# Performance work log

Hardware: AMD Instinct MI355X
Metric: run time of the kernel (lower is better)

Reference implementation:

```python
import jax, jax.numpy as jnp
import numpy as np

N = 10000
E = 160000
H = 4
NEG_SLOPE = 0.2


def _edge_softmax(e, dst):
    # e: [E, H] logits; softmax over edges sharing the same dst node
    m = jax.ops.segment_max(e, dst, num_segments=N)          # [N, H]
    m = jnp.where(jnp.isfinite(m), m, 0.0)
    ex = jnp.exp(e - m[dst])                                  # [E, H]
    den = jax.ops.segment_sum(ex, dst, num_segments=N)       # [N, H]
    return ex / (den[dst] + 1e-9)


def _gat_layer(x, src, dst, W, al, ar, resW, edge=None, We=None, ae=None):
    # x: [N, Fin]; W: [Fin, H, D]; al/ar/ae: [H, D]; resW: [Fin, D]
    feat = jnp.einsum('ni,ihd->nhd', x, W)                    # [N, H, D]
    el = jnp.einsum('nhd,hd->nh', feat, al)                   # [N, H]
    er = jnp.einsum('nhd,hd->nh', feat, ar)                   # [N, H]
    e = el[src] + er[dst]                                     # [E, H]
    if edge is not None:
        ef = jnp.einsum('ei,ihd->ehd', edge, We)              # [E, H, D]
        e = e + jnp.einsum('ehd,hd->eh', ef, ae)
    e = jax.nn.leaky_relu(e, NEG_SLOPE)
    alpha = _edge_softmax(e, dst)                             # [E, H]
    msg = feat[src] * alpha[:, :, None]                       # [E, H, D]
    out = jax.ops.segment_sum(msg, dst, num_segments=N)      # [N, H, D]
    return out.mean(axis=1) + x @ resW                        # [N, D]


def setup_inputs() -> dict:
    key = jax.random.key(0)
    ks = jax.random.split(key, 24)
    node_in, edge_in, hid, out = 128, 64, 128, 256
    s = 0.1
    d = {
        'node_feats': jax.random.normal(ks[0], (N, node_in), jnp.float32),
        'edge_feats': jax.random.normal(ks[1], (E, edge_in), jnp.float32),
        'src': jax.random.randint(ks[2], (E,), 0, N, jnp.int32),
        'dst': jax.random.randint(ks[3], (E,), 0, N, jnp.int32),
        # conv1 (with edge feats): node_in -> hid
        'W1':  s * jax.random.normal(ks[4],  (node_in, H, hid), jnp.float32),
        'We1': s * jax.random.normal(ks[5],  (edge_in, H, hid), jnp.float32),
        'al1': s * jax.random.normal(ks[6],  (H, hid), jnp.float32),
        'ar1': s * jax.random.normal(ks[7],  (H, hid), jnp.float32),
        'ae1': s * jax.random.normal(ks[8],  (H, hid), jnp.float32),
        'res1': s * jax.random.normal(ks[9], (node_in, hid), jnp.float32),
        # conv2: hid -> hid
        'W2':  s * jax.random.normal(ks[10], (hid, H, hid), jnp.float32),
        'al2': s * jax.random.normal(ks[11], (H, hid), jnp.float32),
        'ar2': s * jax.random.normal(ks[12], (H, hid), jnp.float32),
        'res2': s * jax.random.normal(ks[13], (hid, hid), jnp.float32),
        # conv3: hid -> hid
        'W3':  s * jax.random.normal(ks[14], (hid, H, hid), jnp.float32),
        'al3': s * jax.random.normal(ks[15], (H, hid), jnp.float32),
        'ar3': s * jax.random.normal(ks[16], (H, hid), jnp.float32),
        'res3': s * jax.random.normal(ks[17], (hid, hid), jnp.float32),
        # conv4: hid -> out
        'W4':  s * jax.random.normal(ks[18], (hid, H, out), jnp.float32),
        'al4': s * jax.random.normal(ks[19], (H, out), jnp.float32),
        'ar4': s * jax.random.normal(ks[20], (H, out), jnp.float32),
        'res4': s * jax.random.normal(ks[21], (hid, out), jnp.float32),
    }
    return d


def reference(node_feats, edge_feats, src, dst,
              W1, We1, al1, ar1, ae1, res1,
              W2, al2, ar2, res2,
              W3, al3, ar3, res3,
              W4, al4, ar4, res4):
    h = jax.nn.relu(_gat_layer(node_feats, src, dst, W1, al1, ar1, res1,
                               edge=edge_feats, We=We1, ae=ae1))
    h = jax.nn.relu(_gat_layer(h, src, dst, W2, al2, ar2, res2))
    h = jax.nn.relu(_gat_layer(h, src, dst, W3, al3, ar3, res3))
    h = jax.nn.relu(_gat_layer(h, src, dst, W4, al4, ar4, res4))
    return h
```

## Files before the change

kernel.cpp:

```cpp
#include <hip/hip_runtime.h>

#define NN 10000
#define EE 160000

typedef __attribute__((ext_vector_type(8))) short bf16x8;
typedef __attribute__((ext_vector_type(4))) float f32x4;
typedef __attribute__((ext_vector_type(2))) float f32x2;

__device__ __forceinline__ float b2f(unsigned short s) {
    union { unsigned u; float f; } v; v.u = ((unsigned)s) << 16; return v.f;
}
__device__ __forceinline__ short f2b(float f) {
    union { float f; unsigned u; } v; v.f = f;
    unsigned r = v.u + 0x7FFF + ((v.u >> 16) & 1);
    return (short)(r >> 16);
}
__device__ __forceinline__ unsigned char f2q(float f) {
    return (unsigned char)(__builtin_amdgcn_cvt_pk_fp8_f32(f, f, 0, false) & 0xFF);
}

__global__ __launch_bounds__(256) void scan_kernel(const int* __restrict__ counts,
                                                   int* __restrict__ off,
                                                   int* __restrict__ cur, int n) {
    __shared__ int part[256];
// ... 14 lines not shown
        r[q] = v;
        s += v.x + v.y + v.z + v.w;
    }
    part[tid] = s;
    __syncthreads();
    for (int o = 1; o < 256; o <<= 1) {
        int v = (tid >= o) ? part[tid - o] : 0;
        __syncthreads();
        part[tid] += v;
        __syncthreads();
    }
    int run = tid ? part[tid - 1] : 0;
    #pragma unroll
    for (int q = 0; q < 10; ++q) {
        int4 v = r[q], o4;
        o4.x = run; run += v.x;
        o4.y = run; run += v.y;
        o4.z = run; run += v.z;
        o4.w = run; run += v.w;
        int idx = lo + q * 4;
        if (idx + 3 < n) { *(int4*)(off + idx) = o4; *(int4*)(cur + idx) = o4; }
        else if (idx < n) {
            off[idx] = o4.x; cur[idx] = o4.x;
            if (idx + 1 < n) { off[idx + 1] = o4.y; cur[idx + 1] = o4.y; }
            if (idx + 2 < n) { off[idx + 2] = o4.z; cur[idx + 2] = o4.z; }
        }
    }
    if (tid == 255) off[n] = part[255];
}

__global__ __launch_bounds__(256) void fill_extra(const int* __restrict__ src,
                                                  const int* __restrict__ dst,
                                                  int* __restrict__ cur,
                                                  const float* __restrict__ ef,
                                                  const float* __restrict__ vbuf,
                                                  int* __restrict__ ssrc,
                                                  float* __restrict__ extra, int E) {
    __shared__ float vs[256];
    vs[threadIdx.x] = vbuf[threadIdx.x];
    __syncthreads();
    int e = blockIdx.x * 256 + threadIdx.x;
    if (e >= E) return;
    int p = atomicAdd(&cur[dst[e]], 1);
    ssrc[p] = src[e];
    float a0 = 0.f, a1 = 0.f, a2 = 0.f, a3 = 0.f;
    const float4* e4 = (const float4*)(ef + (size_t)e * 64);
    #pragma unroll
    for (int c = 0; c < 16; ++c) {
        float4 x = e4[c];
        int b = c * 16;
        a0 += x.x * vs[b + 0] + x.y * vs[b + 4] + x.z * vs[b + 8] + x.w * vs[b + 12];
        a1 += x.x * vs[b + 1] + x.y * vs[b + 5] + x.z * vs[b + 9] + x.w * vs[b + 13];
        a2 += x.x * vs[b + 2] + x.y * vs[b + 6] + x.z * vs[b + 10] + x.w * vs[b + 14];
        a3 += x.x * vs[b + 3] + x.y * vs[b + 7] + x.z * vs[b + 11] + x.w * vs[b + 15];
    }
    float4 o; o.x = a0; o.y = a1; o.z = a2; o.w = a3;
    *(float4*)(extra + (size_t)p * 4) = o;
}

struct PrepParams {
    const float* tsrc[8];
    short* tdst[8];
    int tN[8];
    int tshift[8];
    int tcum4[9];
    const float* W[4]; const float* al[4]; const float* ar[4];
    short* Wc[4]; int Dl[4]; int base[4];
    const float* We1; const float* ae1; float* vbuf;
    const float* node_feats; short* xb;
    int* counts;
    int bWA, bV, bC, bZ;
};
__global__ __launch_bounds__(256) void prep_kernel(PrepParams P) {
    int blk = blockIdx.x, tid = threadIdx.x;
    if (blk < P.bWA) {
        int t = blk * 256 + tid;
        if (t >= P.tcum4[8]) return;
        int i = 0;
        #pragma unroll
        for (int j = 1; j < 8; ++j) i += (t >= P.tcum4[j]);
        int local = t - P.tcum4[i];
        int N = P.tN[i], sh = P.tshift[i];
        int k = local >> (sh - 2);
        int nq = local & ((N >> 2) - 1);
        float4 v = *(const float4*)(P.tsrc[i] + (size_t)k * N + nq * 4);
        short* d = P.tdst[i] + (size_t)nq * 4 * 128 + k;
        d[0] = f2b(v.x); d[128] = f2b(v.y); d[256] = f2b(v.z); d[384] = f2b(v.w);
    } else if (blk < P.bV) {
        int bl = blk - P.bWA;
        int l = bl >> 7, within = bl & 127;
// ... 76 lines not shown
            int gm = m0 + mt * 16 + r;
            bf16x8 afrag = {};
            if (gm < M) afrag = *(const bf16x8*)(A + (size_t)gm * 128 + k0 + quad * 8);
            acc[mt] = __builtin_amdgcn_mfma_f32_16x16x32_bf16(afrag, bfrag, acc[mt], 0, 0, 0);
        }
    }
    int col = n0 + r;
    #pragma unroll
    for (int mt = 0; mt < 4; ++mt) {
        #pragma unroll
        for (int rr = 0; rr < 4; ++rr) {
            int gm = m0 + mt * 16 + quad * 4 + rr;
            if (gm >= M) continue;
            float v = acc[mt][rr];
            if (col < HD)              featq[(size_t)gm * HD + col] = f2q(v);
            else if (col < HD + D)     y[(size_t)gm * D + (col - HD)] = v;
            else if (col < HD + D + 8) elr[(size_t)gm * 8 + (col - HD - D)] = v;
        }
    }
}

template <int D>
__global__ __launch_bounds__(256) void gemm_fused(const short* __restrict__ A,
                                                  const short* __restrict__ Bt,
                                                  unsigned char* __restrict__ featq,
                                                  float* __restrict__ y,
                                                  float* __restrict__ elr,
                                                  int M) {
    gemm_body<D>(A, Bt, featq, y, elr, M, blockIdx.x, blockIdx.y);
}

__global__ __launch_bounds__(256) void hist_gemm1(const int* __restrict__ dst,
                                                  int* __restrict__ counts,
                                                  const short* __restrict__ A,
                                                  const short* __restrict__ Bt,
                                                  unsigned char* __restrict__ featq,
                                                  float* __restrict__ y,
                                                  float* __restrict__ elr) {
    constexpr int HB = (EE + 255) / 256;
    if (blockIdx.x < HB) {
        int e = blockIdx.x * 256 + threadIdx.x;
        if (e < EE) atomicAdd(&counts[dst[e]], 1);
        return;
    }
    int b = blockIdx.x - HB;
    gemm_body<128>(A, Bt, featq, y, elr, NN, b % 11, b / 11);
}

__device__ __forceinline__ void accum16q(float* a, uint4 v, float w) {
    f32x2 p;
    p = __builtin_amdgcn_cvt_pk_f32_fp8(v.x, false); a[0] += w * p.x; a[1] += w * p.y;
    p = __builtin_amdgcn_cvt_pk_f32_fp8(v.x, true);  a[2] += w * p.x; a[3] += w * p.y;
    p = __builtin_amdgcn_cvt_pk_f32_fp8(v.y, false); a[4] += w * p.x; a[5] += w * p.y;
    p = __builtin_amdgcn_cvt_pk_f32_fp8(v.y, true);  a[6] += w * p.x; a[7] += w * p.y;
    p = __builtin_amdgcn_cvt_pk_f32_fp8(v.z, false); a[8] += w * p.x; a[9] += w * p.y;
    p = __builtin_amdgcn_cvt_pk_f32_fp8(v.z, true);  a[10] += w * p.x; a[11] += w * p.y;
    p = __builtin_amdgcn_cvt_pk_f32_fp8(v.w, false); a[12] += w * p.x; a[13] += w * p.y;
    p = __builtin_amdgcn_cvt_pk_f32_fp8(v.w, true);  a[14] += w * p.x; a[15] += w * p.y;
}

__device__ __forceinline__ float hsel(int h, float s0, float s1, float s2, float s3) {
    return h == 0 ? s0 : h == 1 ? s1 : h == 2 ? s2 : s3;
}

__device__ __forceinline__ void gather128(int T, int deg, int sub, int h, int sidx,
                                          float e0, float e1, float e2, float e3,
                                          const unsigned char* __restrict__ basep,
                                          float acc[16]) {
    int it = 0;
    for (; it + 4 <= T; it += 4) {
        int j0 = 4 * it + sub, j1 = j0 + 4, j2 = j0 + 8, j3 = j0 + 12;
        int c0 = j0 < deg ? j0 : deg - 1;
        int c1 = j1 < deg ? j1 : deg - 1;
        int c2 = j2 < deg ? j2 : deg - 1;
        int c3 = j3 < deg ? j3 : deg - 1;
        float m0 = j0 < deg ? 1.f : 0.f, m1 = j1 < deg ? 1.f : 0.f;
        float m2 = j2 < deg ? 1.f : 0.f, m3 = j3 < deg ? 1.f : 0.f;
        int s0 = __shfl(sidx, c0), s1 = __shfl(sidx, c1);
        int s2 = __shfl(sidx, c2), s3 = __shfl(sidx, c3);
        uint4 v0 = *(const uint4*)(basep + (size_t)s0 * 512);
        uint4 v1 = *(const uint4*)(basep + (size_t)s1 * 512);
        uint4 v2 = *(const uint4*)(basep + (size_t)s2 * 512);
        uint4 v3 = *(const uint4*)(basep + (size_t)s3 * 512);
        float w0 = hsel(h, __shfl(e0, c0), __shfl(e1, c0), __shfl(e2, c0), __shfl(e3, c0)) * m0;
        float w1 = hsel(h, __shfl(e0, c1), __shfl(e1, c1), __shfl(e2, c1), __shfl(e3, c1)) * m1;
        float w2 = hsel(h, __shfl(e0, c2), __shfl(e1, c2), __shfl(e2, c2), __shfl(e3, c2)) * m2;
        float w3 = hsel(h, __shfl(e0, c3), __shfl(e1, c3), __shfl(e2, c3), __shfl(e3, c3)) * m3;
        accum16q(acc, v0, w0); accum16q(acc, v1, w1);
        accum16q(acc, v2, w2); accum16q(acc, v3, w3);
    }
    for (; it < T; ++it) {
        int j0 = 4 * it + sub;
        int c0 = j0 < deg ? j0 : deg - 1;
        float m0 = j0 < deg ? 1.f : 0.f;
        int s0 = __shfl(sidx, c0);
        uint4 v0 = *(const uint4*)(basep + (size_t)s0 * 512);
        float w0 = hsel(h, __shfl(e0, c0), __shfl(e1, c0), __shfl(e2, c0), __shfl(e3, c0)) * m0;
        accum16q(acc, v0, w0);
    }
}

__device__ __forceinline__ void gather256(int T, int deg, int sub, int h, int sidx,
                                          float e0, float e1, float e2, float e3,
                                          const unsigned char* __restrict__ basep,
                                          float acc[16]) {
    int it = 0;
    for (; it + 4 <= T; it += 4) {
        int j0 = 4 * it + sub, j1 = j0 + 4, j2 = j0 + 8, j3 = j0 + 12;
        int c0 = j0 < deg ? j0 : deg - 1;
        int c1 = j1 < deg ? j1 : deg - 1;
        int c2 = j2 < deg ? j2 : deg - 1;
        int c3 = j3 < deg ? j3 : deg - 1;
        float m0 = j0 < deg ? 1.f : 0.f, m1 = j1 < deg ? 1.f : 0.f;
        float m2 = j2 < deg ? 1.f : 0.f, m3 = j3 < deg ? 1.f : 0.f;
        int s0 = __shfl(sidx, c0), s1 = __shfl(sidx, c1);
        int s2 = __shfl(sidx, c2), s3 = __shfl(sidx, c3);
        uint4 v0 = *(const uint4*)(basep + (size_t)s0 * 1024);
        uint4 v1 = *(const uint4*)(basep + (size_t)s1 * 1024);
        uint4 v2 = *(const uint4*)(basep + (size_t)s2 * 1024);
        uint4 v3 = *(const uint4*)(basep + (size_t)s3 * 1024);
        float w0 = hsel(h, __shfl(e0, c0), __shfl(e1, c0), __shfl(e2, c0), __shfl(e3, c0)) * m0;
        float w1 = hsel(h, __shfl(e0, c1), __shfl(e1, c1), __shfl(e2, c1), __shfl(e3, c1)) * m1;
        float w2 = hsel(h, __shfl(e0, c2), __shfl(e1, c2), __shfl(e2, c2), __shfl(e3, c2)) * m2;
        float w3 = hsel(h, __shfl(e0, c3), __shfl(e1, c3), __shfl(e2, c3), __shfl(e3, c3)) * m3;
        accum16q(acc, v0, w0); accum16q(acc, v1, w1);
        accum16q(acc, v2, w2); accum16q(acc, v3, w3);
    }
    for (; it < T; ++it) {
        int j0 = 4 * it + sub;
        int c0 = j0 < deg ? j0 : deg - 1;
        float m0 = j0 < deg ? 1.f : 0.f;
        int s0 = __shfl(sidx, c0);
        uint4 v0 = *(const uint4*)(basep + (size_t)s0 * 1024);
        float w0 = hsel(h, __shfl(e0, c0), __shfl(e1, c0), __shfl(e2, c0), __shfl(e3, c0)) * m0;
        accum16q(acc, v0, w0);
    }
}

#define WAVE_MAX4(m0,m1,m2,m3)                                              \
    _Pragma("unroll")                                                       \
    for (int o = 32; o; o >>= 1) {                                          \
        m0 = fmaxf(m0, __shfl_xor(m0, o)); m1 = fmaxf(m1, __shfl_xor(m1, o));\
        m2 = fmaxf(m2, __shfl_xor(m2, o)); m3 = fmaxf(m3, __shfl_xor(m3, o));\
    }
#define WAVE_SUM4(s0,s1,s2,s3)                                              \
    _Pragma("unroll")                                                       \
    for (int o = 32; o; o >>= 1) {                                          \
        s0 += __shfl_xor(s0, o); s1 += __shfl_xor(s1, o);                   \
        s2 += __shfl_xor(s2, o); s3 += __shfl_xor(s3, o);                   \
    }

template <bool HAS_EXTRA>
__global__ __launch_bounds__(256) void gat128(const unsigned char* __restrict__ featq,
                                              const float* __restrict__ elr,
                                              const float* __restrict__ extra,
                                              const int* __restrict__ ssrc,
                                              const int* __restrict__ off,
                                              const float* __restrict__ yres,
                                              short* __restrict__ ybf) {
    __shared__ float red[2][128];
    int wv = threadIdx.x >> 6, ln = threadIdx.x & 63;
    int slot = wv >> 1, half = wv & 1;
    int n = blockIdx.x * 2 + slot;
    int r0 = off[n], deg = off[n + 1] - r0;
    int g = ln >> 5, l5 = ln & 31;
    int h = l5 >> 3;
    float4 erv = *(const float4*)(elr + (size_t)n * 8 + 4);
    float acc[16];
    #pragma unroll
    for (int i = 0; i < 16; ++i) acc[i] = 0.f;
    float sc0, sc1, sc2, sc3;
    const unsigned char* basep = featq + l5 * 16;
    int sub = half * 2 + g;

    auto logits = [&](int idx, float& a0, float& a1, float& a2, float& a3) {
        int s = ssrc[idx];
        float4 elv = *(const float4*)(elr + (size_t)s * 8);
        a0 = elv.x + erv.x; a1 = elv.y + erv.y; a2 = elv.z + erv.z; a3 = elv.w + erv.w;
        if (HAS_EXTRA) {
            float4 exv = *(const float4*)(extra + (size_t)idx * 4);
            a0 += exv.x; a1 += exv.y; a2 += exv.z; a3 += exv.w;
        }
        a0 = a0 > 0.f ? a0 : 0.2f * a0;
        a1 = a1 > 0.f ? a1 : 0.2f * a1;
        a2 = a2 > 0.f ? a2 : 0.2f * a2;
        a3 = a3 > 0.f ? a3 : 0.2f * a3;
        return s;
    };

    if (deg <= 64) {
        int sidx = 0;
        float a0 = -1e30f, a1 = -1e30f, a2 = -1e30f, a3 = -1e30f;
        if (ln < deg) sidx = logits(r0 + ln, a0, a1, a2, a3);
        float m0 = a0, m1 = a1, m2 = a2, m3 = a3;
        WAVE_MAX4(m0, m1, m2, m3)
        float e0 = 0.f, e1 = 0.f, e2 = 0.f, e3 = 0.f;
        if (ln < deg) {
            e0 = __expf(a0 - m0); e1 = __expf(a1 - m1);
            e2 = __expf(a2 - m2); e3 = __expf(a3 - m3);
        }
        float s0 = e0, s1 = e1, s2 = e2, s3 = e3;
        WAVE_SUM4(s0, s1, s2, s3)
        sc0 = 0.25f / (s0 + 1e-9f); sc1 = 0.25f / (s1 + 1e-9f);
        sc2 = 0.25f / (s2 + 1e-9f); sc3 = 0.25f / (s3 + 1e-9f);
        gather128((deg + 3) >> 2, deg, sub, h, sidx, e0, e1, e2, e3, basep, acc);
    } else {
        float m0 = -1e30f, m1 = -1e30f, m2 = -1e30f, m3 = -1e30f;
        for (int b = 0; b < deg; b += 64) {
            float a0 = -1e30f, a1 = -1e30f, a2 = -1e30f, a3 = -1e30f;
            if (b + ln < deg) logits(r0 + b + ln, a0, a1, a2, a3);
            m0 = fmaxf(m0, a0); m1 = fmaxf(m1, a1); m2 = fmaxf(m2, a2); m3 = fmaxf(m3, a3);
        }
        WAVE_MAX4(m0, m1, m2, m3)
        float s0 = 0.f, s1 = 0.f, s2 = 0.f, s3 = 0.f;
        for (int b = 0; b < deg; b += 64) {
            float a0, a1, a2, a3;
            if (b + ln < deg) {
                logits(r0 + b + ln, a0, a1, a2, a3);
                s0 += __expf(a0 - m0); s1 += __expf(a1 - m1);
                s2 += __expf(a2 - m2); s3 += __expf(a3 - m3);
            }
        }
        WAVE_SUM4(s0, s1, s2, s3)
        sc0 = 0.25f / (s0 + 1e-9f); sc1 = 0.25f / (s1 + 1e-9f);
        sc2 = 0.25f / (s2 + 1e-9f); sc3 = 0.25f / (s3 + 1e-9f);
        for (int b = 0; b < deg; b += 64) {
            int sidx = 0;
            float e0 = 0.f, e1 = 0.f, e2 = 0.f, e3 = 0.f;
            if (b + ln < deg) {
                float a0, a1, a2, a3;
                sidx = logits(r0 + b + ln, a0, a1, a2, a3);
                e0 = __expf(a0 - m0); e1 = __expf(a1 - m1);
                e2 = __expf(a2 - m2); e3 = __expf(a3 - m3);
            }
            int cnt = deg - b; if (cnt > 64) cnt = 64;
            gather128((cnt + 3) >> 2, cnt, sub, h, sidx, e0, e1, e2, e3, basep, acc);
        }
    }

    float scl = hsel(h, sc0, sc1, sc2, sc3);
    float t[16];
    #pragma unroll
    for (int i = 0; i < 16; ++i) {
        float v = acc[i] * scl;
        v += __shfl_xor(v, 32);
        v += __shfl_xor(v, 8);
        v += __shfl_xor(v, 16);
        t[i] = v;
    }
    if (half == 1 && ln < 8) {
        #pragma unroll
        for (int i = 0; i < 16; ++i) red[slot][ln * 16 + i] = t[i];
    }
    __syncthreads();
    if (half == 0 && ln < 8) {
        int d0 = ln * 16;
        const float* yr = yres + (size_t)n * 128 + d0;
        unsigned pk[8];
        #pragma unroll
        for (int q = 0; q < 8; ++q) {
            float ya = yr[2 * q], yb = yr[2 * q + 1];
            float o0 = fmaxf(ya + t[2 * q] + red[slot][d0 + 2 * q], 0.f);
            float o1 = fmaxf(yb + t[2 * q + 1] + red[slot][d0 + 2 * q + 1], 0.f);
            pk[q] = (unsigned short)f2b(o0) | ((unsigned)(unsigned short)f2b(o1) << 16);
        }
        uint4 pa, pb;
        pa.x = pk[0]; pa.y = pk[1]; pa.z = pk[2]; pa.w = pk[3];
        pb.x = pk[4]; pb.y = pk[5]; pb.z = pk[6]; pb.w = pk[7];
        *(uint4*)(ybf + (size_t)n * 128 + d0) = pa;
        *(uint4*)(ybf + (size_t)n * 128 + d0 + 8) = pb;
    }
}

__global__ __launch_bounds__(256) void gat256(const unsigned char* __restrict__ featq,
                                              const float* __restrict__ elr,
                                              const int* __restrict__ ssrc,
                                              const int* __restrict__ off,
                                              const float* __restrict__ yres,
                                              float* __restrict__ yout) {
    __shared__ float red[3][256];
    int wv = threadIdx.x >> 6, ln = threadIdx.x & 63;
    int n = blockIdx.x;
    int r0 = off[n], deg = off[n + 1] - r0;
    int h = ln >> 4;
    float4 erv = *(const float4*)(elr + (size_t)n * 8 + 4);
    float acc[16];
    #pragma unroll
    for (int i = 0; i < 16; ++i) acc[i] = 0.f;
    float sc0, sc1, sc2, sc3;
    const unsigned char* basep = featq + ln * 16;

    auto logits = [&](int idx, float& a0, float& a1, float& a2, float& a3) {
        int s = ssrc[idx];
        float4 elv = *(const float4*)(elr + (size_t)s * 8);
        a0 = elv.x + erv.x; a1 = elv.y + erv.y; a2 = elv.z + erv.z; a3 = elv.w + erv.w;
        a0 = a0 > 0.f ? a0 : 0.2f * a0;
        a1 = a1 > 0.f ? a1 : 0.2f * a1;
        a2 = a2 > 0.f ? a2 : 0.2f * a2;
        a3 = a3 > 0.f ? a3 : 0.2f * a3;
        return s;
    };

    if (deg <= 64) {
        int sidx = 0;
        float a0 = -1e30f, a1 = -1e30f, a2 = -1e30f, a3 = -1e30f;
        if (ln < deg) sidx = logits(r0 + ln, a0, a1, a2, a3);
        float m0 = a0, m1 = a1, m2 = a2, m3 = a3;
        WAVE_MAX4(m0, m1, m2, m3)
        float e0 = 0.f, e1 = 0.f, e2 = 0.f, e3 = 0.f;
        if (ln < deg) {
            e0 = __expf(a0 - m0); e1 = __expf(a1 - m1);
            e2 = __expf(a2 - m2); e3 = __expf(a3 - m3);
        }
        float s0 = e0, s1 = e1, s2 = e2, s3 = e3;
        WAVE_SUM4(s0, s1, s2, s3)
        sc0 = 0.25f / (s0 + 1e-9f); sc1 = 0.25f / (s1 + 1e-9f);
        sc2 = 0.25f / (s2 + 1e-9f); sc3 = 0.25f / (s3 + 1e-9f);
        gather256((deg + 3) >> 2, deg, wv, h, sidx, e0, e1, e2, e3, basep, acc);
    } else {
        float m0 = -1e30f, m1 = -1e30f, m2 = -1e30f, m3 = -1e30f;
        for (int b = 0; b < deg; b += 64) {
            float a0 = -1e30f, a1 = -1e30f, a2 = -1e30f, a3 = -1e30f;
            if (b + ln < deg) logits(r0 + b + ln, a0, a1, a2, a3);
            m0 = fmaxf(m0, a0); m1 = fmaxf(m1, a1); m2 = fmaxf(m2, a2); m3 = fmaxf(m3, a3);
        }
        WAVE_MAX4(m0, m1, m2, m3)
        float s0 = 0.f, s1 = 0.f, s2 = 0.f, s3 = 0.f;
        for (int b = 0; b < deg; b += 64) {
            float a0, a1, a2, a3;
            if (b + ln < deg) {
                logits(r0 + b + ln, a0, a1, a2, a3);
                s0 += __expf(a0 - m0); s1 += __expf(a1 - m1);
                s2 += __expf(a2 - m2); s3 += __expf(a3 - m3);
            }
        }
        WAVE_SUM4(s0, s1, s2, s3)
        sc0 = 0.25f / (s0 + 1e-9f); sc1 = 0.25f / (s1 + 1e-9f);
        sc2 = 0.25f / (s2 + 1e-9f); sc3 = 0.25f / (s3 + 1e-9f);
        for (int b = 0; b < deg; b += 64) {
            int sidx = 0;
            float e0 = 0.f, e1 = 0.f, e2 = 0.f, e3 = 0.f;
            if (b + ln < deg) {
                float a0, a1, a2, a3;
                sidx = logits(r0 + b + ln, a0, a1, a2, a3);
                e0 = __expf(a0 - m0); e1 = __expf(a1 - m1);
                e2 = __expf(a2 - m2); e3 = __expf(a3 - m3);
            }
            int cnt = deg - b; if (cnt > 64) cnt = 64;
            gather256((cnt + 3) >> 2, cnt, wv, h, sidx, e0, e1, e2, e3, basep, acc);
        }
    }

    float scl = hsel(h, sc0, sc1, sc2, sc3);
    float t[16];
    #pragma unroll
    for (int i = 0; i < 16; ++i) {
        float v = acc[i] * scl;
        v += __shfl_xor(v, 16);
        v += __shfl_xor(v, 32);
        t[i] = v;
    }
    if (wv > 0 && ln < 16) {
        #pragma unroll
        for (int i = 0; i < 16; ++i) red[wv - 1][ln * 16 + i] = t[i];
    }
    __syncthreads();
    if (wv == 0 && ln < 16) {
        int d0 = ln * 16;
        const float* yr = yres + (size_t)n * 256 + d0;
        float* yo = yout + (size_t)n * 256 + d0;
        #pragma unroll
        for (int q = 0; q < 4; ++q) {
            float4 ya = *(const float4*)(yr + 4 * q);
            float4 ov;
            ov.x = fmaxf(ya.x + t[4 * q + 0] + red[0][d0 + 4 * q + 0] + red[1][d0 + 4 * q + 0] + red[2][d0 + 4 * q + 0], 0.f);
            ov.y = fmaxf(ya.y + t[4 * q + 1] + red[0][d0 + 4 * q + 1] + red[1][d0 + 4 * q + 1] + red[2][d0 + 4 * q + 1], 0.f);
            ov.z = fmaxf(ya.z + t[4 * q + 2] + red[0][d0 + 4 * q + 2] + red[1][d0 + 4 * q + 2] + red[2][d0 + 4 * q + 2], 0.f);
            ov.w = fmaxf(ya.w + t[4 * q + 3] + red[0][d0 + 4 * q + 3] + red[1][d0 + 4 * q + 3] + red[2][d0 + 4 * q + 3], 0.f);
            *(float4*)(yo + 4 * q) = ov;
        }
    }
}

extern "C" void kernel_launch(void* const* d_in, const int* in_sizes, int n_in,
                              void* d_out, int out_size, void* d_ws, size_t ws_size,
                              hipStream_t stream) {
    const float* node_feats = (const float*)d_in[0];
    const float* edge_feats = (const float*)d_in[1];
    const int*   src        = (const int*)d_in[2];
    const int*   dst        = (const int*)d_in[3];
    const float* W1   = (const float*)d_in[4];
    const float* We1  = (const float*)d_in[5];
    const float* al1  = (const float*)d_in[6];
    const float* ar1  = (const float*)d_in[7];
    const float* ae1  = (const float*)d_in[8];
    const float* res1 = (const float*)d_in[9];
    const float* W2   = (const float*)d_in[10];
    const float* al2  = (const float*)d_in[11];
    const float* ar2  = (const float*)d_in[12];
    const float* res2 = (const float*)d_in[13];
    const float* W3   = (const float*)d_in[14];
    const float* al3  = (const float*)d_in[15];
    const float* ar3  = (const float*)d_in[16];
    const float* res3 = (const float*)d_in[17];
    const float* W4   = (const float*)d_in[18];
    const float* al4  = (const float*)d_in[19];
    const float* ar4  = (const float*)d_in[20];
    const float* res4 = (const float*)d_in[21];

    char* ws = (char*)d_ws;
    auto alloc = [&](size_t bytes) -> char* {
        char* p = ws;
        ws += (bytes + 255) & ~(size_t)255;
        return p;
    };
    int*   counts  = (int*)alloc((size_t)NN * 4);
    int*   offsets = (int*)alloc((size_t)(NN + 1) * 4);
    int*   cursor  = (int*)alloc((size_t)(NN + 1) * 4);
    int*   ssrc    = (int*)alloc((size_t)EE * 4);
    unsigned char* featq = (unsigned char*)alloc((size_t)NN * 1024);
    float* xA      = (float*)alloc((size_t)NN * 128 * 4);
    short* xb      = (short*)alloc((size_t)NN * 128 * 2);
    float* elr     = (float*)alloc((size_t)NN * 8 * 4);
    float* extra   = (float*)alloc((size_t)EE * 4 * 4);
    float* vbuf    = (float*)alloc(1024);
    short* Wc1     = (short*)alloc((size_t)704 * 128 * 2);
    short* Wc2     = (short*)alloc((size_t)704 * 128 * 2);
    short* Wc3     = (short*)alloc((size_t)704 * 128 * 2);
    short* Wc4     = (short*)alloc((size_t)1344 * 128 * 2);

    PrepParams P;
    P.tsrc[0] = W1;   P.tdst[0] = Wc1;              P.tN[0] = 512;  P.tshift[0] = 9;
    P.tsrc[1] = W2;   P.tdst[1] = Wc2;              P.tN[1] = 512;  P.tshift[1] = 9;
    P.tsrc[2] = W3;   P.tdst[2] = Wc3;              P.tN[2] = 512;  P.tshift[2] = 9;
    P.tsrc[3] = W4;   P.tdst[3] = Wc4;              P.tN[3] = 1024; P.tshift[3] = 10;
    P.tsrc[4] = res1; P.tdst[4] = Wc1 + 512 * 128;  P.tN[4] = 128;  P.tshift[4] = 7;
    P.tsrc[5] = res2; P.tdst[5] = Wc2 + 512 * 128;  P.tN[5] = 128;  P.tshift[5] = 7;
    P.tsrc[6] = res3; P.tdst[6] = Wc3 + 512 * 128;  P.tN[6] = 128;  P.tshift[6] = 7;
    P.tsrc[7] = res4; P.tdst[7] = Wc4 + 1024 * 128; P.tN[7] = 256;  P.tshift[7] = 8;
    P.tcum4[0] = 0;
    for (int i = 0; i < 8; ++i) P.tcum4[i + 1] = P.tcum4[i] + P.tN[i] * 128 / 4;
    P.W[0] = W1; P.W[1] = W2; P.W[2] = W3; P.W[3] = W4;
    P.al[0] = al1; P.al[1] = al2; P.al[2] = al3; P.al[3] = al4;
    P.ar[0] = ar1; P.ar[1] = ar2; P.ar[2] = ar3; P.ar[3] = ar4;
    P.Wc[0] = Wc1; P.Wc[1] = Wc2; P.Wc[2] = Wc3; P.Wc[3] = Wc4;
    P.Dl[0] = 128; P.Dl[1] = 128; P.Dl[2] = 128; P.Dl[3] = 256;
    P.base[0] = 640; P.base[1] = 640; P.base[2] = 640; P.base[3] = 1280;
    P.We1 = We1; P.ae1 = ae1; P.vbuf = vbuf;
    P.node_feats = node_feats; P.xb = xb;
    P.counts = counts;
    P.bWA = (P.tcum4[8] + 255) / 256;
    P.bV  = P.bWA + 512;
    P.bC  = P.bV + 16;
    P.bZ  = P.bC + (NN * 32 + 255) / 256;
    int nblk = P.bZ + (NN / 4 + 255) / 256;
    prep_kernel<<<nblk, 256, 0, stream>>>(P);

    float* out = (float*)d_out;
    dim3 g128(11, (NN + 63) / 64);
    dim3 g256(21, (NN + 63) / 64);
    constexpr int HB = (EE + 255) / 256;

    hist_gemm1<<<HB + 11 * ((NN + 63) / 64), 256, 0, stream>>>(dst, counts, xb, Wc1,
                                                               featq, xA, elr);
    scan_kernel<<<1, 256, 0, stream>>>(counts, offsets, cursor, NN);
    fill_extra<<<(EE + 255) / 256, 256, 0, stream>>>(src, dst, cursor, edge_feats,
                                                     vbuf, ssrc, extra, EE);

    gat128<true><<<NN / 2, 256, 0, stream>>>(featq, elr, extra, ssrc, offsets, xA, xb);
    gemm_fused<128><<<g128, 256, 0, stream>>>(xb, Wc2, featq, xA, elr, NN);
    gat128<false><<<NN / 2, 256, 0, stream>>>(featq, elr, nullptr, ssrc, offsets, xA, xb);
    gemm_fused<128><<<g128, 256, 0, stream>>>(xb, Wc3, featq, xA, elr, NN);
    gat128<false><<<NN / 2, 256, 0, stream>>>(featq, elr, nullptr, ssrc, offsets, xA, xb);
    gemm_fused<256><<<g256, 256, 0, stream>>>(xb, Wc4, featq, out, elr, NN);
    gat256<<<NN, 256, 0, stream>>>(featq, elr, ssrc, offsets, out, out);
}
```

Baseline: 414.7 us.

## Remap GAT aggregation to one wave per node with per-head lane groups

Restructures the gat128 and gat256 aggregation kernels so each node is handled by one wave (gat128) or two waves (gat256) rather than two or four. Lanes are split into per-head groups of 16, each computing the softmax for its own head, which removes the four-way head select and the shared-memory cross-wave reduction in gat128. The edge-feature projection moves out of the scatter kernel into the histogram part of the first fused kernel, so fill_extra becomes a plain permuted copy. This adds an extra E×4 float buffer and serial per-lane loops over edges for high-degree nodes.

```diff
diff --git a/kernel.cpp b/kernel.cpp
--- a/kernel.cpp
+++ b/kernel.cpp
@@ -70,30 +70,14 @@
 __global__ __launch_bounds__(256) void fill_extra(const int* __restrict__ src,
                                                   const int* __restrict__ dst,
                                                   int* __restrict__ cur,
-                                                  const float* __restrict__ ef,
-                                                  const float* __restrict__ vbuf,
+                                                  const float* __restrict__ extraU,
                                                   int* __restrict__ ssrc,
                                                   float* __restrict__ extra, int E) {
-    __shared__ float vs[256];
-    vs[threadIdx.x] = vbuf[threadIdx.x];
-    __syncthreads();
     int e = blockIdx.x * 256 + threadIdx.x;
     if (e >= E) return;
     int p = atomicAdd(&cur[dst[e]], 1);
     ssrc[p] = src[e];
-    float a0 = 0.f, a1 = 0.f, a2 = 0.f, a3 = 0.f;
-    const float4* e4 = (const float4*)(ef + (size_t)e * 64);
-    #pragma unroll
-    for (int c = 0; c < 16; ++c) {
-        float4 x = e4[c];
-        int b = c * 16;
-        a0 += x.x * vs[b + 0] + x.y * vs[b + 4] + x.z * vs[b + 8] + x.w * vs[b + 12];
-        a1 += x.x * vs[b + 1] + x.y * vs[b + 5] + x.z * vs[b + 9] + x.w * vs[b + 13];
-        a2 += x.x * vs[b + 2] + x.y * vs[b + 6] + x.z * vs[b + 10] + x.w * vs[b + 14];
-        a3 += x.x * vs[b + 3] + x.y * vs[b + 7] + x.z * vs[b + 11] + x.w * vs[b + 15];
-    }
-    float4 o; o.x = a0; o.y = a1; o.z = a2; o.w = a3;
-    *(float4*)(extra + (size_t)p * 4) = o;
+    *(float4*)(extra + (size_t)p * 4) = *(const float4*)(extraU + (size_t)e * 4);
 }
 
 struct PrepParams {
@@ -236,6 +220,9 @@
 
 __global__ __launch_bounds__(256) void hist_gemm1(const int* __restrict__ dst,
                                                   int* __restrict__ counts,
+                                                  const float* __restrict__ ef,
+                                                  const float* __restrict__ vbuf,
+                                                  float* __restrict__ extraU,
                                                   const short* __restrict__ A,
                                                   const short* __restrict__ Bt,
                                                   unsigned char* __restrict__ featq,
@@ -243,14 +230,39 @@
                                                   float* __restrict__ elr) {
     constexpr int HB = (EE + 255) / 256;
     if (blockIdx.x < HB) {
+        __shared__ float vs[256];
+        vs[threadIdx.x] = vbuf[threadIdx.x];
+        __syncthreads();
         int e = blockIdx.x * 256 + threadIdx.x;
-        if (e < EE) atomicAdd(&counts[dst[e]], 1);
+        if (e < EE) {
+            atomicAdd(&counts[dst[e]], 1);
+            float a0 = 0.f, a1 = 0.f, a2 = 0.f, a3 = 0.f;
+            const float4* e4 = (const float4*)(ef + (size_t)e * 64);
+            #pragma unroll
+            for (int c = 0; c < 16; ++c) {
+                float4 x = e4[c];
+                int b = c * 16;
+                a0 += x.x * vs[b + 0] + x.y * vs[b + 4] + x.z * vs[b + 8] + x.w * vs[b + 12];
+                a1 += x.x * vs[b + 1] + x.y * vs[b + 5] + x.z * vs[b + 9] + x.w * vs[b + 13];
+                a2 += x.x * vs[b + 2] + x.y * vs[b + 6] + x.z * vs[b + 10] + x.w * vs[b + 14];
+                a3 += x.x * vs[b + 3] + x.y * vs[b + 7] + x.z * vs[b + 11] + x.w * vs[b + 15];
+            }
+            float4 o; o.x = a0; o.y = a1; o.z = a2; o.w = a3;
+            *(float4*)(extraU + (size_t)e * 4) = o;
+        }
         return;
     }
     int b = blockIdx.x - HB;
     gemm_body<128>(A, Bt, featq, y, elr, NN, b % 11, b / 11);
 }
 
+__device__ __forceinline__ void accum8q(float* a, uint2 v, float w) {
+    f32x2 p;
+    p = __builtin_amdgcn_cvt_pk_f32_fp8(v.x, false); a[0] += w * p.x; a[1] += w * p.y;
+    p = __builtin_amdgcn_cvt_pk_f32_fp8(v.x, true);  a[2] += w * p.x; a[3] += w * p.y;
+    p = __builtin_amdgcn_cvt_pk_f32_fp8(v.y, false); a[4] += w * p.x; a[5] += w * p.y;
+    p = __builtin_amdgcn_cvt_pk_f32_fp8(v.y, true);  a[6] += w * p.x; a[7] += w * p.y;
+}
 __device__ __forceinline__ void accum16q(float* a, uint4 v, float w) {
     f32x2 p;
     p = __builtin_amdgcn_cvt_pk_f32_fp8(v.x, false); a[0] += w * p.x; a[1] += w * p.y;
@@ -263,96 +275,39 @@
     p = __builtin_amdgcn_cvt_pk_f32_fp8(v.w, true);  a[14] += w * p.x; a[15] += w * p.y;
 }
 
-__device__ __forceinline__ float hsel(int h, float s0, float s1, float s2, float s3) {
-    return h == 0 ? s0 : h == 1 ? s1 : h == 2 ? s2 : s3;
-}
-
-__device__ __forceinline__ void gather128(int T, int deg, int sub, int h, int sidx,
-                                          float e0, float e1, float e2, float e3,
-                                          const unsigned char* __restrict__ basep,
-                                          float acc[16]) {
-    int it = 0;
-    for (; it + 4 <= T; it += 4) {
-        int j0 = 4 * it + sub, j1 = j0 + 4, j2 = j0 + 8, j3 = j0 + 12;
-        int c0 = j0 < deg ? j0 : deg - 1;
-        int c1 = j1 < deg ? j1 : deg - 1;
-        int c2 = j2 < deg ? j2 : deg - 1;
-        int c3 = j3 < deg ? j3 : deg - 1;
-        float m0 = j0 < deg ? 1.f : 0.f, m1 = j1 < deg ? 1.f : 0.f;
-        float m2 = j2 < deg ? 1.f : 0.f, m3 = j3 < deg ? 1.f : 0.f;
-        int s0 = __shfl(sidx, c0), s1 = __shfl(sidx, c1);
-        int s2 = __shfl(sidx, c2), s3 = __shfl(sidx, c3);
-        uint4 v0 = *(const uint4*)(basep + (size_t)s0 * 512);
-        uint4 v1 = *(const uint4*)(basep + (size_t)s1 * 512);
-        uint4 v2 = *(const uint4*)(basep + (size_t)s2 * 512);
-        uint4 v3 = *(const uint4*)(basep + (size_t)s3 * 512);
-        float w0 = hsel(h, __shfl(e0, c0), __shfl(e1, c0), __shfl(e2, c0), __shfl(e3, c0)) * m0;
-        float w1 = hsel(h, __shfl(e0, c1), __shfl(e1, c1), __shfl(e2, c1), __shfl(e3, c1)) * m1;
-        float w2 = hsel(h, __shfl(e0, c2), __shfl(e1, c2), __shfl(e2, c2), __shfl(e3, c2)) * m2;
-        float w3 = hsel(h, __shfl(e0, c3), __shfl(e1, c3), __shfl(e2, c3), __shfl(e3, c3)) * m3;
-        accum16q(acc, v0, w0); accum16q(acc, v1, w1);
-        accum16q(acc, v2, w2); accum16q(acc, v3, w3);
-    }
-    for (; it < T; ++it) {
-        int j0 = 4 * it + sub;
-        int c0 = j0 < deg ? j0 : deg - 1;
-        float m0 = j0 < deg ? 1.f : 0.f;
-        int s0 = __shfl(sidx, c0);
-        uint4 v0 = *(const uint4*)(basep + (size_t)s0 * 512);
-        float w0 = hsel(h, __shfl(e0, c0), __shfl(e1, c0), __shfl(e2, c0), __shfl(e3, c0)) * m0;
-        accum16q(acc, v0, w0);
-    }
-}
-
-__device__ __forceinline__ void gather256(int T, int deg, int sub, int h, int sidx,
-                                          float e0, float e1, float e2, float e3,
-                                          const unsigned char* __restrict__ basep,
-                                          float acc[16]) {
-    int it = 0;
-    for (; it + 4 <= T; it += 4) {
-        int j0 = 4 * it + sub, j1 = j0 + 4, j2 = j0 + 8, j3 = j0 + 12;
-        int c0 = j0 < deg ? j0 : deg - 1;
-        int c1 = j1 < deg ? j1 : deg - 1;
-        int c2 = j2 < deg ? j2 : deg - 1;
-        int c3 = j3 < deg ? j3 : deg - 1;
-        float m0 = j0 < deg ? 1.f : 0.f, m1 = j1 < deg ? 1.f : 0.f;
-        float m2 = j2 < deg ? 1.f : 0.f, m3 = j3 < deg ? 1.f : 0.f;
-        int s0 = __shfl(sidx, c0), s1 = __shfl(sidx, c1);
-        int s2 = __shfl(sidx, c2), s3 = __shfl(sidx, c3);
-        uint4 v0 = *(const uint4*)(basep + (size_t)s0 * 1024);
-        uint4 v1 = *(const uint4*)(basep + (size_t)s1 * 1024);
-        uint4 v2 = *(const uint4*)(basep + (size_t)s2 * 1024);
-        uint4 v3 = *(const uint4*)(basep + (size_t)s3 * 1024);
-        float w0 = hsel(h, __shfl(e0, c0), __shfl(e1, c0), __shfl(e2, c0), __shfl(e3, c0)) * m0;
-        float w1 = hsel(h, __shfl(e0, c1), __shfl(e1, c1), __shfl(e2, c1), __shfl(e3, c1)) * m1;
-        float w2 = hsel(h, __shfl(e0, c2), __shfl(e1, c2), __shfl(e2, c2), __shfl(e3, c2)) * m2;
-        float w3 = hsel(h, __shfl(e0, c3), __shfl(e1, c3), __shfl(e2, c3), __shfl(e3, c3)) * m3;
-        accum16q(acc, v0, w0); accum16q(acc, v1, w1);
-        accum16q(acc, v2, w2); accum16q(acc, v3, w3);
-    }
-    for (; it < T; ++it) {
-        int j0 = 4 * it + sub;
-        int c0 = j0 < deg ? j0 : deg - 1;
-        float m0 = j0 < deg ? 1.f : 0.f;
-        int s0 = __shfl(sidx, c0);
-        uint4 v0 = *(const uint4*)(basep + (size_t)s0 * 1024);
-        float w0 = hsel(h, __shfl(e0, c0), __shfl(e1, c0), __shfl(e2, c0), __shfl(e3, c0)) * m0;
-        accum16q(acc, v0, w0);
-    }
-}
-
-#define WAVE_MAX4(m0,m1,m2,m3)                                              \
-    _Pragma("unroll")                                                       \
-    for (int o = 32; o; o >>= 1) {                                          \
-        m0 = fmaxf(m0, __shfl_xor(m0, o)); m1 = fmaxf(m1, __shfl_xor(m1, o));\
-        m2 = fmaxf(m2, __shfl_xor(m2, o)); m3 = fmaxf(m3, __shfl_xor(m3, o));\
-    }
-#define WAVE_SUM4(s0,s1,s2,s3)                                              \
-    _Pragma("unroll")                                                       \
-    for (int o = 32; o; o >>= 1) {                                          \
-        s0 += __shfl_xor(s0, o); s1 += __shfl_xor(s1, o);                   \
-        s2 += __shfl_xor(s2, o); s3 += __shfl_xor(s3, o);                   \
-    }
+template <bool HAS_EXTRA>
+__device__ __forceinline__ void softmax64(int r0, int deg, int h, int jh, float erh,
+                                          const float* __restrict__ elr,
+                                          const float* __restrict__ extra,
+                                          const int* __restrict__ ssrc,
+                                          float& ev0, float& ev1, float& ev2, float& ev3,
+                                          int& sx0, int& sx1, int& sx2, int& sx3,
+                                          float& sc) {
+    float a0 = -1e30f, a1 = -1e30f, a2 = -1e30f, a3 = -1e30f;
+    sx0 = sx1 = sx2 = sx3 = 0;
+    auto lg = [&](int j, int& sx, float& a) {
+        if (j < deg) {
+            int idx = r0 + j;
+            sx = ssrc[idx];
+            float v = elr[(size_t)sx * 8 + h] + erh;
+            if (HAS_EXTRA) v += extra[(size_t)idx * 4 + h];
+            a = v > 0.f ? v : 0.2f * v;
+        }
+    };
+    lg(jh, sx0, a0);
+    if (deg > 16) lg(jh + 16, sx1, a1);
+    if (deg > 32) lg(jh + 32, sx2, a2);
+    if (deg > 48) lg(jh + 48, sx3, a3);
+    float m = fmaxf(fmaxf(a0, a1), fmaxf(a2, a3));
+    #pragma unroll
+    for (int o = 1; o < 16; o <<= 1) m = fmaxf(m, __shfl_xor(m, o));
+    ev0 = __expf(a0 - m); ev1 = __expf(a1 - m);
+    ev2 = __expf(a2 - m); ev3 = __expf(a3 - m);
+    float ss = ev0 + ev1 + ev2 + ev3;
+    #pragma unroll
+    for (int o = 1; o < 16; o <<= 1) ss += __shfl_xor(ss, o);
+    sc = 0.25f / (ss + 1e-9f);
+}
 
 template <bool HAS_EXTRA>
 __global__ __launch_bounds__(256) void gat128(const unsigned char* __restrict__ featq,
@@ -362,117 +317,78 @@
                                               const int* __restrict__ off,
                                               const float* __restrict__ yres,
                                               short* __restrict__ ybf) {
-    __shared__ float red[2][128];
     int wv = threadIdx.x >> 6, ln = threadIdx.x & 63;
-    int slot = wv >> 1, half = wv & 1;
-    int n = blockIdx.x * 2 + slot;
+    int n = blockIdx.x * 4 + wv;
     int r0 = off[n], deg = off[n + 1] - r0;
-    int g = ln >> 5, l5 = ln & 31;
-    int h = l5 >> 3;
-    float4 erv = *(const float4*)(elr + (size_t)n * 8 + 4);
-    float acc[16];
-    #pragma unroll
-    for (int i = 0; i < 16; ++i) acc[i] = 0.f;
-    float sc0, sc1, sc2, sc3;
-    const unsigned char* basep = featq + l5 * 16;
-    int sub = half * 2 + g;
-
-    auto logits = [&](int idx, float& a0, float& a1, float& a2, float& a3) {
-        int s = ssrc[idx];
-        float4 elv = *(const float4*)(elr + (size_t)s * 8);
-        a0 = elv.x + erv.x; a1 = elv.y + erv.y; a2 = elv.z + erv.z; a3 = elv.w + erv.w;
-        if (HAS_EXTRA) {
-            float4 exv = *(const float4*)(extra + (size_t)idx * 4);
-            a0 += exv.x; a1 += exv.y; a2 += exv.z; a3 += exv.w;
-        }
-        a0 = a0 > 0.f ? a0 : 0.2f * a0;
-        a1 = a1 > 0.f ? a1 : 0.2f * a1;
-        a2 = a2 > 0.f ? a2 : 0.2f * a2;
-        a3 = a3 > 0.f ? a3 : 0.2f * a3;
-        return s;
-    };
+    int h = ln >> 4, jh = ln & 15;
+    float erh = elr[(size_t)n * 8 + 4 + h];
+    float acc[8];
+    #pragma unroll
+    for (int i = 0; i < 8; ++i) acc[i] = 0.f;
+    const unsigned char* basep = featq + ln * 8;
+    float sc;
 
     if (deg <= 64) {
-        int sidx = 0;
-        float a0 = -1e30f, a1 = -1e30f, a2 = -1e30f, a3 = -1e30f;
-        if (ln < deg) sidx = logits(r0 + ln, a0, a1, a2, a3);
-        float m0 = a0, m1 = a1, m2 = a2, m3 = a3;
-        WAVE_MAX4(m0, m1, m2, m3)
-        float e0 = 0.f, e1 = 0.f, e2 = 0.f, e3 = 0.f;
-        if (ln < deg) {
-            e0 = __expf(a0 - m0); e1 = __expf(a1 - m1);
-            e2 = __expf(a2 - m2); e3 = __expf(a3 - m3);
-        }
-        float s0 = e0, s1 = e1, s2 = e2, s3 = e3;
-        WAVE_SUM4(s0, s1, s2, s3)
-        sc0 = 0.25f / (s0 + 1e-9f); sc1 = 0.25f / (s1 + 1e-9f);
-        sc2 = 0.25f / (s2 + 1e-9f); sc3 = 0.25f / (s3 + 1e-9f);
-        gather128((deg + 3) >> 2, deg, sub, h, sidx, e0, e1, e2, e3, basep, acc);
+        float ev0, ev1, ev2, ev3;
+        int sx0, sx1, sx2, sx3;
+        softmax64<HAS_EXTRA>(r0, deg, h, jh, erh, elr, extra, ssrc,
+                             ev0, ev1, ev2, ev3, sx0, sx1, sx2, sx3, sc);
+        auto step = [&](int c) {
+            int slot = c >> 4;
+            float ee = slot == 0 ? ev0 : slot == 1 ? ev1 : slot == 2 ? ev2 : ev3;
+            int   si = slot == 0 ? sx0 : slot == 1 ? sx1 : slot == 2 ? sx2 : sx3;
+            float w = __shfl(ee, (h << 4) | (c & 15));
+            int   s = __shfl(si, c & 15);
+            uint2 v = *(const uint2*)(basep + (size_t)s * 512);
+            accum8q(acc, v, w);
+        };
+        int c = 0;
+        for (; c + 4 <= deg; c += 4) {
+            step(c); step(c + 1); step(c + 2); step(c + 3);
+        }
+        for (; c < deg; ++c) step(c);
     } else {
-        float m0 = -1e30f, m1 = -1e30f, m2 = -1e30f, m3 = -1e30f;
-        for (int b = 0; b < deg; b += 64) {
-            float a0 = -1e30f, a1 = -1e30f, a2 = -1e30f, a3 = -1e30f;
-            if (b + ln < deg) logits(r0 + b + ln, a0, a1, a2, a3);
-            m0 = fmaxf(m0, a0); m1 = fmaxf(m1, a1); m2 = fmaxf(m2, a2); m3 = fmaxf(m3, a3);
-        }
-        WAVE_MAX4(m0, m1, m2, m3)
-        float s0 = 0.f, s1 = 0.f, s2 = 0.f, s3 = 0.f;
-        for (int b = 0; b < deg; b += 64) {
-            float a0, a1, a2, a3;
-            if (b + ln < deg) {
-                logits(r0 + b + ln, a0, a1, a2, a3);
-                s0 += __expf(a0 - m0); s1 += __expf(a1 - m1);
-                s2 += __expf(a2 - m2); s3 += __expf(a3 - m3);
-            }
-        }
-        WAVE_SUM4(s0, s1, s2, s3)
-        sc0 = 0.25f / (s0 + 1e-9f); sc1 = 0.25f / (s1 + 1e-9f);
-        sc2 = 0.25f / (s2 + 1e-9f); sc3 = 0.25f / (s3 + 1e-9f);
-        for (int b = 0; b < deg; b += 64) {
-            int sidx = 0;
-            float e0 = 0.f, e1 = 0.f, e2 = 0.f, e3 = 0.f;
-            if (b + ln < deg) {
-                float a0, a1, a2, a3;
-                sidx = logits(r0 + b + ln, a0, a1, a2, a3);
-                e0 = __expf(a0 - m0); e1 = __expf(a1 - m1);
-                e2 = __expf(a2 - m2); e3 = __expf(a3 - m3);
-            }
-            int cnt = deg - b; if (cnt > 64) cnt = 64;
-            gather128((cnt + 3) >> 2, cnt, sub, h, sidx, e0, e1, e2, e3, basep, acc);
-        }
-    }
-
-    float scl = hsel(h, sc0, sc1, sc2, sc3);
-    float t[16];
-    #pragma unroll
-    for (int i = 0; i < 16; ++i) {
-        float v = acc[i] * scl;
+        auto lgt = [&](int c) {
+            int s = ssrc[r0 + c];
+            float v = elr[(size_t)s * 8 + h] + erh;
+            if (HAS_EXTRA) v += extra[(size_t)(r0 + c) * 4 + h];
+            return v > 0.f ? v : 0.2f * v;
+        };
+        float m = -1e30f;
+        for (int c = 0; c < deg; ++c) m = fmaxf(m, lgt(c));
+        float ss = 0.f;
+        for (int c = 0; c < deg; ++c) ss += __expf(lgt(c) - m);
+        sc = 0.25f / (ss + 1e-9f);
+        for (int c = 0; c < deg; ++c) {
+            float w = __expf(lgt(c) - m);
+            int s = ssrc[r0 + c];
+            uint2 v = *(const uint2*)(basep + (size_t)s * 512);
+            accum8q(acc, v, w);
+        }
+    }
+
+    float t[8];
+    #pragma unroll
+    for (int i = 0; i < 8; ++i) {
+        float v = acc[i] * sc;
+        v += __shfl_xor(v, 16);
         v += __shfl_xor(v, 32);
-        v += __shfl_xor(v, 8);
-        v += __shfl_xor(v, 16);
         t[i] = v;
     }
-    if (half == 1 && ln < 8) {
-        #pragma unroll
-        for (int i = 0; i < 16; ++i) red[slot][ln * 16 + i] = t[i];
-    }
-    __syncthreads();
-    if (half == 0 && ln < 8) {
-        int d0 = ln * 16;
-        const float* yr = yres + (size_t)n * 128 + d0;
-        unsigned pk[8];
-        #pragma unroll
-        for (int q = 0; q < 8; ++q) {
-            float ya = yr[2 * q], yb = yr[2 * q + 1];
-            float o0 = fmaxf(ya + t[2 * q] + red[slot][d0 + 2 * q], 0.f);
-            float o1 = fmaxf(yb + t[2 * q + 1] + red[slot][d0 + 2 * q + 1], 0.f);
-            pk[q] = (unsigned short)f2b(o0) | ((unsigned)(unsigned short)f2b(o1) << 16);
-        }
-        uint4 pa, pb;
-        pa.x = pk[0]; pa.y = pk[1]; pa.z = pk[2]; pa.w = pk[3];
-        pb.x = pk[4]; pb.y = pk[5]; pb.z = pk[6]; pb.w = pk[7];
-        *(uint4*)(ybf + (size_t)n * 128 + d0) = pa;
-        *(uint4*)(ybf + (size_t)n * 128 + d0 + 8) = pb;
+    if (ln < 16) {
+        const float* yr = yres + (size_t)n * 128 + ln * 8;
+        float4 y0 = *(const float4*)yr;
+        float4 y1 = *(const float4*)(yr + 4);
+        float o0 = fmaxf(y0.x + t[0], 0.f), o1 = fmaxf(y0.y + t[1], 0.f);
+        float o2 = fmaxf(y0.z + t[2], 0.f), o3 = fmaxf(y0.w + t[3], 0.f);
+        float o4 = fmaxf(y1.x + t[4], 0.f), o5 = fmaxf(y1.y + t[5], 0.f);
+        float o6 = fmaxf(y1.z + t[6], 0.f), o7 = fmaxf(y1.w + t[7], 0.f);
+        uint4 pa;
+        pa.x = (unsigned short)f2b(o0) | ((unsigned)(unsigned short)f2b(o1) << 16);
+        pa.y = (unsigned short)f2b(o2) | ((unsigned)(unsigned short)f2b(o3) << 16);
+        pa.z = (unsigned short)f2b(o4) | ((unsigned)(unsigned short)f2b(o5) << 16);
+        pa.w = (unsigned short)f2b(o6) | ((unsigned)(unsigned short)f2b(o7) << 16);
+        *(uint4*)(ybf + (size_t)n * 128 + ln * 8) = pa;
     }
 }
 
@@ -482,105 +398,83 @@
                                               const int* __restrict__ off,
                                               const float* __restrict__ yres,
                                               float* __restrict__ yout) {
-    __shared__ float red[3][256];
+    __shared__ float red[2][16 * 17];
     int wv = threadIdx.x >> 6, ln = threadIdx.x & 63;
-    int n = blockIdx.x;
+    int slot = wv >> 1, half = wv & 1;
+    int n = blockIdx.x * 2 + slot;
     int r0 = off[n], deg = off[n + 1] - r0;
-    int h = ln >> 4;
-    float4 erv = *(const float4*)(elr + (size_t)n * 8 + 4);
+    int h = ln >> 4, jh = ln & 15;
+    float erh = elr[(size_t)n * 8 + 4 + h];
     float acc[16];
     #pragma unroll
     for (int i = 0; i < 16; ++i) acc[i] = 0.f;
-    float sc0, sc1, sc2, sc3;
     const unsigned char* basep = featq + ln * 16;
-
-    auto logits = [&](int idx, float& a0, float& a1, float& a2, float& a3) {
-        int s = ssrc[idx];
-        float4 elv = *(const float4*)(elr + (size_t)s * 8);
-        a0 = elv.x + erv.x; a1 = elv.y + erv.y; a2 = elv.z + erv.z; a3 = elv.w + erv.w;
-        a0 = a0 > 0.f ? a0 : 0.2f * a0;
-        a1 = a1 > 0.f ? a1 : 0.2f * a1;
-        a2 = a2 > 0.f ? a2 : 0.2f * a2;
-        a3 = a3 > 0.f ? a3 : 0.2f * a3;
-        return s;
-    };
+    float sc;
 
     if (deg <= 64) {
-        int sidx = 0;
-        float a0 = -1e30f, a1 = -1e30f, a2 = -1e30f, a3 = -1e30f;
-        if (ln < deg) sidx = logits(r0 + ln, a0, a1, a2, a3);
-        float m0 = a0, m1 = a1, m2 = a2, m3 = a3;
-        WAVE_MAX4(m0, m1, m2, m3)
-        float e0 = 0.f, e1 = 0.f, e2 = 0.f, e3 = 0.f;
-        if (ln < deg) {
-            e0 = __expf(a0 - m0); e1 = __expf(a1 - m1);
-            e2 = __expf(a2 - m2); e3 = __expf(a3 - m3);
-        }
-        float s0 = e0, s1 = e1, s2 = e2, s3 = e3;
-        WAVE_SUM4(s0, s1, s2, s3)
-        sc0 = 0.25f / (s0 + 1e-9f); sc1 = 0.25f / (s1 + 1e-9f);
-        sc2 = 0.25f / (s2 + 1e-9f); sc3 = 0.25f / (s3 + 1e-9f);
-        gather256((deg + 3) >> 2, deg, wv, h, sidx, e0, e1, e2, e3, basep, acc);
+        float ev0, ev1, ev2, ev3;
+        int sx0, sx1, sx2, sx3;
+        softmax64<false>(r0, deg, h, jh, erh, elr, nullptr, ssrc,
+                         ev0, ev1, ev2, ev3, sx0, sx1, sx2, sx3, sc);
+        auto step = [&](int c) {
+            int sl = c >> 4;
+            float ee = sl == 0 ? ev0 : sl == 1 ? ev1 : sl == 2 ? ev2 : ev3;
+            int   si = sl == 0 ? sx0 : sl == 1 ? sx1 : sl == 2 ? sx2 : sx3;
+            float w = __shfl(ee, (h << 4) | (c & 15));
+            int   s = __shfl(si, c & 15);
+            uint4 v = *(const uint4*)(basep + (size_t)s * 1024);
+            accum16q(acc, v, w);
+        };
+        int T = (deg - half + 1) >> 1;
+        int it = 0;
+        for (; it + 4 <= T; it += 4) {
+            step(2 * it + half); step(2 * it + 2 + half);
+            step(2 * it + 4 + half); step(2 * it + 6 + half);
+        }
+        for (; it < T; ++it) step(2 * it + half);
     } else {
-        float m0 = -1e30f, m1 = -1e30f, m2 = -1e30f, m3 = -1e30f;
-        for (int b = 0; b < deg; b += 64) {
-            float a0 = -1e30f, a1 = -1e30f, a2 = -1e30f, a3 = -1e30f;
-            if (b + ln < deg) logits(r0 + b + ln, a0, a1, a2, a3);
-            m0 = fmaxf(m0, a0); m1 = fmaxf(m1, a1); m2 = fmaxf(m2, a2); m3 = fmaxf(m3, a3);
-        }
-        WAVE_MAX4(m0, m1, m2, m3)
-        float s0 = 0.f, s1 = 0.f, s2 = 0.f, s3 = 0.f;
-        for (int b = 0; b < deg; b += 64) {
-            float a0, a1, a2, a3;
-            if (b + ln < deg) {
-                logits(r0 + b + ln, a0, a1, a2, a3);
-                s0 += __expf(a0 - m0); s1 += __expf(a1 - m1);
-                s2 += __expf(a2 - m2); s3 += __expf(a3 - m3);
-            }
-        }
-        WAVE_SUM4(s0, s1, s2, s3)
-        sc0 = 0.25f / (s0 + 1e-9f); sc1 = 0.25f / (s1 + 1e-9f);
-        sc2 = 0.25f / (s2 + 1e-9f); sc3 = 0.25f / (s3 + 1e-9f);
-        for (int b = 0; b < deg; b += 64) {
-            int sidx = 0;
-            float e0 = 0.f, e1 = 0.f, e2 = 0.f, e3 = 0.f;
-            if (b + ln < deg) {
-                float a0, a1, a2, a3;
-                sidx = logits(r0 + b + ln, a0, a1, a2, a3);
-                e0 = __expf(a0 - m0); e1 = __expf(a1 - m1);
-                e2 = __expf(a2 - m2); e3 = __expf(a3 - m3);
-            }
-            int cnt = deg - b; if (cnt > 64) cnt = 64;
-            gather256((cnt + 3) >> 2, cnt, wv, h, sidx, e0, e1, e2, e3, basep, acc);
-        }
-    }
-
-    float scl = hsel(h, sc0, sc1, sc2, sc3);
+        auto lgt = [&](int c) {
+            int s = ssrc[r0 + c];
+            float v = elr[(size_t)s * 8 + h] + erh;
+            return v > 0.f ? v : 0.2f * v;
+        };
+        float m = -1e30f;
+        for (int c = 0; c < deg; ++c) m = fmaxf(m, lgt(c));
+        float ss = 0.f;
+        for (int c = 0; c < deg; ++c) ss += __expf(lgt(c) - m);
+        sc = 0.25f / (ss + 1e-9f);
+        for (int c = half; c < deg; c += 2) {
+            float w = __expf(lgt(c) - m);
+            int s = ssrc[r0 + c];
+            uint4 v = *(const uint4*)(basep + (size_t)s * 1024);
+            accum16q(acc, v, w);
+        }
+    }
+
     float t[16];
     #pragma unroll
     for (int i = 0; i < 16; ++i) {
-        float v = acc[i] * scl;
+        float v = acc[i] * sc;
         v += __shfl_xor(v, 16);
         v += __shfl_xor(v, 32);
         t[i] = v;
     }
-    if (wv > 0 && ln < 16) {
-        #pragma unroll
-        for (int i = 0; i < 16; ++i) red[wv - 1][ln * 16 + i] = t[i];
+    if (half == 1 && ln < 16) {
+        #pragma unroll
+        for (int i = 0; i < 16; ++i) red[slot][ln * 17 + i] = t[i];
     }
     __syncthreads();
-    if (wv == 0 && ln < 16) {
-        int d0 = ln * 16;
-        const float* yr = yres + (size_t)n * 256 + d0;
-        float* yo = yout + (size_t)n * 256 + d0;
+    if (half == 0 && ln < 16) {
+        const float* yr = yres + (size_t)n * 256 + ln * 16;
+        float* yo = yout + (size_t)n * 256 + ln * 16;
         #pragma unroll
         for (int q = 0; q < 4; ++q) {
             float4 ya = *(const float4*)(yr + 4 * q);
             float4 ov;
-            ov.x = fmaxf(ya.x + t[4 * q + 0] + red[0][d0 + 4 * q + 0] + red[1][d0 + 4 * q + 0] + red[2][d0 + 4 * q + 0], 0.f);
-            ov.y = fmaxf(ya.y + t[4 * q + 1] + red[0][d0 + 4 * q + 1] + red[1][d0 + 4 * q + 1] + red[2][d0 + 4 * q + 1], 0.f);
-            ov.z = fmaxf(ya.z + t[4 * q + 2] + red[0][d0 + 4 * q + 2] + red[1][d0 + 4 * q + 2] + red[2][d0 + 4 * q + 2], 0.f);
-            ov.w = fmaxf(ya.w + t[4 * q + 3] + red[0][d0 + 4 * q + 3] + red[1][d0 + 4 * q + 3] + red[2][d0 + 4 * q + 3], 0.f);
+            ov.x = fmaxf(ya.x + t[4 * q + 0] + red[slot][ln * 17 + 4 * q + 0], 0.f);
+            ov.y = fmaxf(ya.y + t[4 * q + 1] + red[slot][ln * 17 + 4 * q + 1], 0.f);
+            ov.z = fmaxf(ya.z + t[4 * q + 2] + red[slot][ln * 17 + 4 * q + 2], 0.f);
+            ov.w = fmaxf(ya.w + t[4 * q + 3] + red[slot][ln * 17 + 4 * q + 3], 0.f);
             *(float4*)(yo + 4 * q) = ov;
         }
     }
@@ -627,6 +521,7 @@
     short* xb      = (short*)alloc((size_t)NN * 128 * 2);
     float* elr     = (float*)alloc((size_t)NN * 8 * 4);
     float* extra   = (float*)alloc((size_t)EE * 4 * 4);
+    float* extraU  = (float*)alloc((size_t)EE * 4 * 4);
     float* vbuf    = (float*)alloc(1024);
     short* Wc1     = (short*)alloc((size_t)704 * 128 * 2);
     short* Wc2     = (short*)alloc((size_t)704 * 128 * 2);
@@ -665,17 +560,17 @@
     dim3 g256(21, (NN + 63) / 64);
     constexpr int HB = (EE + 255) / 256;
 
-    hist_gemm1<<<HB + 11 * ((NN + 63) / 64), 256, 0, stream>>>(dst, counts, xb, Wc1,
-                                                               featq, xA, elr);
+    hist_gemm1<<<HB + 11 * ((NN + 63) / 64), 256, 0, stream>>>(
+        dst, counts, edge_feats, vbuf, extraU, xb, Wc1, featq, xA, elr);
     scan_kernel<<<1, 256, 0, stream>>>(counts, offsets, cursor, NN);
-    fill_extra<<<(EE + 255) / 256, 256, 0, stream>>>(src, dst, cursor, edge_feats,
-                                                     vbuf, ssrc, extra, EE);
-
-    gat128<true><<<NN / 2, 256, 0, stream>>>(featq, elr, extra, ssrc, offsets, xA, xb);
+    fill_extra<<<(EE + 255) / 256, 256, 0, stream>>>(src, dst, cursor, extraU,
+                                                     ssrc, extra, EE);
+
+    gat128<true><<<NN / 4, 256, 0, stream>>>(featq, elr, extra, ssrc, offsets, xA, xb);
     gemm_fused<128><<<g128, 256, 0, stream>>>(xb, Wc2, featq, xA, elr, NN);
-    gat128<false><<<NN / 2, 256, 0, stream>>>(featq, elr, nullptr, ssrc, offsets, xA, xb);
+    gat128<false><<<NN / 4, 256, 0, stream>>>(featq, elr, nullptr, ssrc, offsets, xA, xb);
     gemm_fused<128><<<g128, 256, 0, stream>>>(xb, Wc3, featq, xA, elr, NN);
-    gat128<false><<<NN / 2, 256, 0, stream>>>(featq, elr, nullptr, ssrc, offsets, xA, xb);
+    gat128<false><<<NN / 4, 256, 0, stream>>>(featq, elr, nullptr, ssrc, offsets, xA, xb);
     gemm_fused<256><<<g256, 256, 0, stream>>>(xb, Wc4, featq, out, elr, NN);
-    gat256<<<NN, 256, 0, stream>>>(featq, elr, ssrc, offsets, out, out);
-}
+    gat256<<<NN / 2, 256, 0, stream>>>(featq, elr, ssrc, offsets, out, out);
+}
```

After: 536.0 us. 29.2% more time.
